# Optimization experiments

Measured on AMD Instinct MI355X. Metric: run time of the kernel, lower is better.

## Reference

```python
import jax, jax.numpy as jnp
import numpy as np

SCALE = 64 ** (-0.5)


def setup_inputs() -> dict:
    key = jax.random.key(0)
    ks = jax.random.split(key, 6)
    B, C, D, N = 2, 1024, 64, 128
    w_std = C ** (-0.5)
    return {
        "lidar": jax.random.normal(ks[0], (B, C, D, N), dtype=jnp.float32),
        "cam": jax.random.normal(ks[1], (B, C, D, N), dtype=jnp.float32),
        "Wq": jax.random.normal(ks[2], (C, C), dtype=jnp.float32) * w_std,
        "Wk": jax.random.normal(ks[3], (C, C), dtype=jnp.float32) * w_std,
        "Wv": jax.random.normal(ks[4], (C, C), dtype=jnp.float32) * w_std,
        "Wo": jax.random.normal(ks[5], (C, C), dtype=jnp.float32) * w_std,
    }


def _proj(W, x):
    # 1x1 Conv1d over flattened (D*N) positions == channel matmul, bias=False
    return jnp.einsum('oc,bcdn->bodn', W, x)


def reference(lidar, cam, Wq, Wk, Wv, Wo):
    q = _proj(Wq, lidar)  # [B, C, D, Ni]
    k = _proj(Wk, cam)    # [B, C, D, Nj]
    v = _proj(Wv, cam)    # [B, C, D, Nj]
    # contract over D (head-dim-like axis); scores per (batch, channel)
    dots = jnp.einsum('bhdi,bhdj->bhij', q, k) * SCALE  # [B, C, Ni, Nj]
    att = jax.nn.softmax(dots, axis=-1)
    # einsum 'a b i c,a b j c->a b j i': contract over cam positions
    out = jnp.einsum('bhic,bhjc->bhji', att, v)  # [B, C, D, Ni]
    out = jax.nn.gelu(_proj(Wo, out), approximate=False)
    return out
```

## Files before the change

kernel.cpp:

```cpp
#include <hip/hip_runtime.h>
#include <math.h>

#define CH  1024
#define PPB 8192

typedef __attribute__((ext_vector_type(8))) short short8;
typedef __attribute__((ext_vector_type(4))) float f32x4;

__device__ __forceinline__ ushort f2bf(float x) {
    uint u = __float_as_uint(x);
    return (ushort)((u + 0x7FFFu + ((u >> 16) & 1u)) >> 16);
}
__device__ __forceinline__ float bf2f(ushort u) {
    return __uint_as_float(((uint)u) << 16);
}
__device__ __forceinline__ void gload16(const void* g, const void* l) {
    __builtin_amdgcn_global_load_lds((const __attribute__((address_space(1))) void*)g,
                                     (__attribute__((address_space(3))) void*)l, 16, 0, 0);
}

__global__ __launch_bounds__(256) void prep(const float* __restrict__ lidar,
                                            const float* __restrict__ cam,
                                            const float* __restrict__ Wq,
                                            const float* __restrict__ Wk,
                                            const float* __restrict__ Wv,
                                            const float* __restrict__ Wo,
                                            ushort* __restrict__ wdst,
                                            ushort* __restrict__ lidT,
                                            ushort* __restrict__ camT)
{
    __shared__ float T[64][65];
    const int blk = blockIdx.x;
    const int tid = threadIdx.x;

    if (blk < 2048) {
        const int y = blk >> 9;
        const int x = blk & 511;
        const float* w = (y == 0) ? Wq : (y == 1) ? Wk : (y == 2) ? Wv : Wo;
        ushort* o = wdst + (size_t)y * (1u << 20);
        const int idx = (x * 256 + tid) * 8;
        const float4 v0 = *(const float4*)(w + idx);
        const float4 v1 = *(const float4*)(w + idx + 4);
        ushort4 o0, o1;
        o0.x = f2bf(v0.x); o0.y = f2bf(v0.y); o0.z = f2bf(v0.z); o0.w = f2bf(v0.w);
        o1.x = f2bf(v1.x); o1.y = f2bf(v1.y); o1.z = f2bf(v1.z); o1.w = f2bf(v1.w);
        *(ushort4*)(o + idx)     = o0;
        *(ushort4*)(o + idx + 4) = o1;
        return;
    }

    const int t = blk - 2048;
    const bool isLid = (t < 4096);
    const int tt = isLid ? t : t - 4096;
    const float* in = isLid ? lidar : cam;
    ushort* out = isLid ? lidT : camT;

    const int p0 = (tt & 127) * 64;
    const int c0 = ((tt >> 7) & 15) * 64;
    const int b  = tt >> 11;
    const int rc = tid >> 4;
    const int rp = (tid & 15) * 4;

    #pragma unroll
    for (int pass = 0; pass < 4; ++pass) {
        const int c = pass * 16 + rc;
        const size_t base = ((size_t)(b * CH + c0 + c)) * PPB + p0 + rp;
        const float4 v = *(const float4*)(in + base);
        T[c][rp] = v.x; T[c][rp + 1] = v.y; T[c][rp + 2] = v.z; T[c][rp + 3] = v.w;
    }
    __syncthreads();
    #pragma unroll
    for (int pass = 0; pass < 4; ++pass) {
        const int p = pass * 16 + rc;
        ushort4 o;
        o.x = f2bf(T[rp + 0][p]); o.y = f2bf(T[rp + 1][p]);
        o.z = f2bf(T[rp + 2][p]); o.w = f2bf(T[rp + 3][p]);
        *(ushort4*)(out + ((size_t)(b * PPB + p0 + p)) * CH + c0 + rp) = o;
    }
}

__global__ __launch_bounds__(256) void transpose_ao(const ushort* __restrict__ in_,
                                                    ushort* __restrict__ out)
{
    __shared__ float T[64][65];
    const int p0 = blockIdx.x * 64;
    const int c0 = blockIdx.y * 64;
    const int b  = blockIdx.z;
    const int t  = threadIdx.x;
    const int rc = t >> 4;
    const int rp = (t & 15) * 4;

    #pragma unroll
    for (int pass = 0; pass < 4; ++pass) {
        const int c = pass * 16 + rc;
        const size_t base = ((size_t)(b * CH + c0 + c)) * PPB + p0 + rp;
        const ushort4 v = *(const ushort4*)(in_ + base);
        T[c][rp]     = bf2f(v.x); T[c][rp + 1] = bf2f(v.y);
        T[c][rp + 2] = bf2f(v.z); T[c][rp + 3] = bf2f(v.w);
    }
    __syncthreads();
    #pragma unroll
    for (int pass = 0; pass < 4; ++pass) {
        const int p = pass * 16 + rc;
        const int prow = p * 128 + blockIdx.x;
        ushort4 o;
        o.x = f2bf(T[rp + 0][p]); o.y = f2bf(T[rp + 1][p]);
        o.z = f2bf(T[rp + 2][p]); o.w = f2bf(T[rp + 3][p]);
        *(ushort4*)(out + ((size_t)(b * PPB + prow)) * CH + c0 + rp) = o;
    }
}

__global__ __launch_bounds__(256) void gemm_qkv(const ushort* __restrict__ W3,
                                                const ushort* __restrict__ lidT,
                                                const ushort* __restrict__ camT,
                                                ushort* __restrict__ out3)
{
    __shared__ ushort As[2][128 * 32];
    __shared__ ushort Bs[2][128 * 32];

    const int bid = blockIdx.x;
    const int sid = (bid & 7) * 384 + (bid >> 3);
    const int g   = sid >> 10;
    const int r0  = sid & 1023;
    const int bm  = r0 & 7;
    const int bn  = r0 >> 3;
    const int m0  = bm * 128;
    const int n0g = bn * 128;
    const int b   = bn >> 6;
    const int p0  = (bn & 63) * 128;
    const int i0  = (bn & 63) * 2;

    const ushort* A  = W3 + (size_t)g * (1u << 20);
    const ushort* Bt = (g == 0) ? lidT : camT;
    const bool remap = (g < 2);
    ushort* Cout = out3 + (size_t)g * ((size_t)16 << 20);

    const int tid = threadIdx.x;
    const int w   = tid >> 6;
    const int l   = tid & 63;
    const int wr  = w >> 1, wc = w & 1;

    f32x4 acc[4][4];
    #pragma unroll
    for (int i = 0; i < 4; ++i)
        #pragma unroll
        for (int j = 0; j < 4; ++j) acc[i][j] = (f32x4)(0.0f);

    auto stage = [&](int buf, int kt) {
        const int k0 = kt * 32;
        #pragma unroll
        for (int i = 0; i < 2; ++i) {
            const int c  = w * 2 + i;
            const int rr = c * 16 + (l >> 2);
            const int ke = k0 + (l & 3) * 8;
            gload16(A + (size_t)(m0 + rr) * CH + ke, &As[buf][c * 512]);
            size_t brow;
            if (remap) brow = (size_t)b * PPB + (size_t)(rr & 63) * 128 + i0 + (rr >> 6);
            else       brow = (size_t)(n0g + rr);
            gload16(Bt + brow * CH + ke, &Bs[buf][c * 512]);
        }
    };

    stage(0, 0);
    int buf = 0;
    const int ks = (l >> 4) * 8;
    const int fr = l & 15;
    for (int kt = 0; kt < 32; ++kt) {
        __syncthreads();
        if (kt + 1 < 32) stage(buf ^ 1, kt + 1);
        short8 af[4], bfr[4];
        #pragma unroll
        for (int fm = 0; fm < 4; ++fm)
            af[fm] = *reinterpret_cast<const short8*>(
                &As[buf][(wr * 64 + fm * 16 + fr) * 32 + ks]);
        #pragma unroll
        for (int fn = 0; fn < 4; ++fn)
            bfr[fn] = *reinterpret_cast<const short8*>(
                &Bs[buf][(wc * 64 + fn * 16 + fr) * 32 + ks]);
        #pragma unroll
        for (int fm = 0; fm < 4; ++fm)
            #pragma unroll
            for (int fn = 0; fn < 4; ++fn)
                acc[fm][fn] = __builtin_amdgcn_mfma_f32_16x16x32_bf16(
                    af[fm], bfr[fn], acc[fm][fn], 0, 0, 0);
        buf ^= 1;
    }

    const int rq = l >> 4;
    #pragma unroll
    for (int fm = 0; fm < 4; ++fm)
        #pragma unroll
        for (int fn = 0; fn < 4; ++fn)
            #pragma unroll
            for (int r = 0; r < 4; ++r) {
                const int m = m0 + wr * 64 + fm * 16 + rq * 4 + r;
                const int n = wc * 64 + fn * 16 + fr;
                const size_t off = (size_t)b * CH * PPB + (size_t)m * PPB + p0 + n;
                ((ushort*)Cout)[off] = f2bf(acc[fm][fn][r]);
            }
}

__global__ __launch_bounds__(256) void gemm_wo(const ushort* __restrict__ A,
                                               const ushort* __restrict__ Bt,
                                               float* __restrict__ Cout)
{
    __shared__ ushort As[2][128 * 32];
    __shared__ ushort Bs[2][128 * 32];

    const int bid = blockIdx.x;
    const int sid = (bid & 7) * 128 + (bid >> 3);
    const int bm  = sid & 7;
    const int bn  = sid >> 3;
    const int m0  = bm * 128;
    const int n0g = bn * 128;
    const int b   = bn >> 6;
    const int p0  = (bn & 63) * 128;

    const int tid = threadIdx.x;
    const int w   = tid >> 6;
    const int l   = tid & 63;
    const int wr  = w >> 1, wc = w & 1;

    f32x4 acc[4][4];
    #pragma unroll
    for (int i = 0; i < 4; ++i)
        #pragma unroll
        for (int j = 0; j < 4; ++j) acc[i][j] = (f32x4)(0.0f);

    auto stage = [&](int buf, int kt) {
        const int k0 = kt * 32;
        #pragma unroll
        for (int i = 0; i < 2; ++i) {
            const int c  = w * 2 + i;
            const int rr = c * 16 + (l >> 2);
            const int ke = k0 + (l & 3) * 8;
            gload16(A  + (size_t)(m0 + rr) * CH + ke, &As[buf][c * 512]);
            gload16(Bt + (size_t)(n0g + rr) * CH + ke, &Bs[buf][c * 512]);
        }
    };

    stage(0, 0);
    int buf = 0;
    const int ks = (l >> 4) * 8;
    const int fr = l & 15;
    for (int kt = 0; kt < 32; ++kt) {
        __syncthreads();
        if (kt + 1 < 32) stage(buf ^ 1, kt + 1);
        short8 af[4], bfr[4];
        #pragma unroll
        for (int fm = 0; fm < 4; ++fm)
            af[fm] = *reinterpret_cast<const short8*>(
                &As[buf][(wr * 64 + fm * 16 + fr) * 32 + ks]);
        #pragma unroll
        for (int fn = 0; fn < 4; ++fn)
            bfr[fn] = *reinterpret_cast<const short8*>(
                &Bs[buf][(wc * 64 + fn * 16 + fr) * 32 + ks]);
        #pragma unroll
        for (int fm = 0; fm < 4; ++fm)
            #pragma unroll
            for (int fn = 0; fn < 4; ++fn)
                acc[fm][fn] = __builtin_amdgcn_mfma_f32_16x16x32_bf16(
                    af[fm], bfr[fn], acc[fm][fn], 0, 0, 0);
        buf ^= 1;
    }

    const int rq = l >> 4;
    #pragma unroll
    for (int fm = 0; fm < 4; ++fm)
        #pragma unroll
        for (int fn = 0; fn < 4; ++fn)
            #pragma unroll
            for (int r = 0; r < 4; ++r) {
                const int m = m0 + wr * 64 + fm * 16 + rq * 4 + r;
                const int n = wc * 64 + fn * 16 + fr;
                const float vv = acc[fm][fn][r];
                const size_t off = (size_t)b * CH * PPB + (size_t)m * PPB + p0 + n;
                Cout[off] = 0.5f * vv * (1.0f + erff(vv * 0.70710678118654752f));
            }
}

__global__ __launch_bounds__(256, 2) void attn_mfma(const ushort* __restrict__ qt,
                                                    const ushort* __restrict__ kt,
                                                    const ushort* __restrict__ vn,
                                                    ushort* __restrict__ ot)
{
    __shared__ ushort Qs[8192];
    __shared__ ushort Ks[8192];
    __shared__ ushort Vs[8192];
    __shared__ ushort Ps[16384];

    const int bh  = blockIdx.x;
    const int tid = threadIdx.x;
    const int w   = tid >> 6;
    const int l   = tid & 63;
    const int hi  = l >> 4;
    const int fr  = l & 15;
    const size_t base = (size_t)bh * 8192;

    {
        const int lr = l >> 3, lb = l & 7;
        const int vr = l >> 4, vbk = l & 15;
        #pragma unroll
        for (int q = 0; q < 4; ++q) {
            const int ch = w * 4 + q;
            const int i  = ch * 8 + lr;
            gload16(qt + base + i * 64 + ((lb ^ (i & 7)) << 3), &Qs[ch * 512]);
            gload16(kt + base + i * 64 + ((lb ^ (i & 7)) << 3), &Ks[ch * 512]);
            const int d  = ch * 4 + vr;
            gload16(vn + base + d * 128 + ((vbk ^ (d & 15)) << 3), &Vs[ch * 512]);
        }
    }
    __syncthreads();

    const int i0w = w * 32;
    f32x4 accS[2][8];
    #pragma unroll
    for (int a = 0; a < 2; ++a)
        #pragma unroll
        for (int bjj = 0; bjj < 8; ++bjj) accS[a][bjj] = (f32x4)(0.0f);

    #pragma unroll
    for (int kk = 0; kk < 2; ++kk) {
        const int blk = kk * 4 + hi;
        short8 aq[2];
        #pragma unroll
        for (int fm = 0; fm < 2; ++fm) {
            const int i = i0w + fm * 16 + fr;
            aq[fm] = *(const short8*)&Qs[i * 64 + ((blk ^ (i & 7)) << 3)];
        }
        #pragma unroll
        for (int fn = 0; fn < 8; ++fn) {
            const int j = fn * 16 + fr;
            const short8 bk = *(const short8*)&Ks[j * 64 + ((blk ^ (j & 7)) << 3)];
            #pragma unroll
            for (int fm = 0; fm < 2; ++fm)
                accS[fm][fn] = __builtin_amdgcn_mfma_f32_16x16x32_bf16(
                    aq[fm], bk, accS[fm][fn], 0, 0, 0);
        }
    }

    const float CS = 0.125f * 1.44269504088896341f;
    #pragma unroll
    for (int fm = 0; fm < 2; ++fm) {
        #pragma unroll
        for (int r = 0; r < 4; ++r) {
            float mx = accS[fm][0][r];
            #pragma unroll
            for (int fn = 1; fn < 8; ++fn) mx = fmaxf(mx, accS[fm][fn][r]);
            #pragma unroll
            for (int msk = 1; msk <= 8; msk <<= 1) mx = fmaxf(mx, __shfl_xor(mx, msk, 64));
            float e[8], sum = 0.f;
            #pragma unroll
            for (int fn = 0; fn < 8; ++fn) {
                e[fn] = exp2f((accS[fm][fn][r] - mx) * CS);
                sum += e[fn];
            }
            #pragma unroll
            for (int msk = 1; msk <= 8; msk <<= 1) sum += __shfl_xor(sum, msk, 64);
            const float is = 1.0f / sum;
            const int i = i0w + fm * 16 + hi * 4 + r;
            #pragma unroll
            for (int fn = 0; fn < 8; ++fn) {
                const int j = fn * 16 + fr;
                Ps[i * 128 + (((j >> 3) ^ (i & 15)) << 3) + (j & 7)] = f2bf(e[fn] * is);
            }
        }
    }

    f32x4 accO[2][4];
    #pragma unroll
    for (int a = 0; a < 2; ++a)
        #pragma unroll
        for (int bjj = 0; bjj < 4; ++bjj) accO[a][bjj] = (f32x4)(0.0f);

    #pragma unroll
    for (int ks2 = 0; ks2 < 4; ++ks2) {
        const int blk = ks2 * 4 + hi;
        short8 ap[2];
        #pragma unroll
        for (int fm = 0; fm < 2; ++fm) {
            const int i = i0w + fm * 16 + fr;
            ap[fm] = *(const short8*)&Ps[i * 128 + ((blk ^ (i & 15)) << 3)];
        }
        #pragma unroll
        for (int fn2 = 0; fn2 < 4; ++fn2) {
            const int d = fn2 * 16 + fr;
            const short8 bv = *(const short8*)&Vs[d * 128 + ((blk ^ (d & 15)) << 3)];
            #pragma unroll
            for (int fm = 0; fm < 2; ++fm)
                accO[fm][fn2] = __builtin_amdgcn_mfma_f32_16x16x32_bf16(
                    ap[fm], bv, accO[fm][fn2], 0, 0, 0);
        }
    }

    #pragma unroll
    for (int fm = 0; fm < 2; ++fm)
        #pragma unroll
        for (int fn2 = 0; fn2 < 4; ++fn2)
            #pragma unroll
            for (int r = 0; r < 4; ++r) {
                const int i = i0w + fm * 16 + hi * 4 + r;
                const int d = fn2 * 16 + fr;
                ot[base + i * 64 + d] = f2bf(accO[fm][fn2][r]);
            }
}

extern "C" void kernel_launch(void* const* d_in, const int* in_sizes, int n_in,
                              void* d_out, int out_size, void* d_ws, size_t ws_size,
                              hipStream_t stream)
{
    const float* lidar = (const float*)d_in[0];
    const float* cam   = (const float*)d_in[1];
    const float* Wq    = (const float*)d_in[2];
    const float* Wk    = (const float*)d_in[3];
    const float* Wv    = (const float*)d_in[4];
    const float* Wo    = (const float*)d_in[5];

    ushort* ws = (ushort*)d_ws;
    const size_t M1 = (size_t)1 << 20;
    const size_t TT = (size_t)16 << 20;
    ushort* Wob  = ws + 3 * M1;
    ushort* lidT = ws + 4 * M1;
    ushort* camT = lidT + TT;
    ushort* qb   = camT + TT;
    ushort* aoT  = lidT;

    const dim3 blk(256);
    prep<<<dim3(10240), blk, 0, stream>>>(lidar, cam, Wq, Wk, Wv, Wo, ws, lidT, camT);

    gemm_qkv<<<dim3(3072), blk, 0, stream>>>(ws, lidT, camT, qb);

    attn_mfma<<<dim3(2048), blk, 0, stream>>>(qb, qb + TT, qb + 2 * TT, qb);

    transpose_ao<<<dim3(128, 16, 2), blk, 0, stream>>>(qb, aoT);

    gemm_wo<<<dim3(1024), blk, 0, stream>>>(Wob, aoT, (float*)d_out);
}
```

Measured before the change: 289.8 us.

## Replace both projection GEMMs with a 256x256-tile swizzled, software-pipelined MFMA kernel

After: 268.3 us. 7.4% less time.

```diff
diff --git a/kernel.cpp b/kernel.cpp
--- a/kernel.cpp
+++ b/kernel.cpp
@@ -110,172 +110,147 @@
     }
 }
 
-__global__ __launch_bounds__(256) void gemm_qkv(const ushort* __restrict__ W3,
-                                                const ushort* __restrict__ lidT,
-                                                const ushort* __restrict__ camT,
-                                                ushort* __restrict__ out3)
+template <int IS_WO>
+__global__ __launch_bounds__(512, 2) void gemm256(const ushort* __restrict__ W3,
+                                                  const ushort* __restrict__ lidT,
+                                                  const ushort* __restrict__ camT,
+                                                  void* __restrict__ outp)
 {
-    __shared__ ushort As[2][128 * 32];
-    __shared__ ushort Bs[2][128 * 32];
+    __shared__ __align__(16) ushort sh[65536];
+    char* shb = (char*)sh;
 
     const int bid = blockIdx.x;
-    const int sid = (bid & 7) * 384 + (bid >> 3);
-    const int g   = sid >> 10;
-    const int r0  = sid & 1023;
-    const int bm  = r0 & 7;
-    const int bn  = r0 >> 3;
-    const int m0  = bm * 128;
-    const int n0g = bn * 128;
-    const int b   = bn >> 6;
-    const int p0  = (bn & 63) * 128;
-    const int i0  = (bn & 63) * 2;
-
+    int g, bm, bn;
+    if (IS_WO) {
+        const int sid = (bid & 7) * 32 + (bid >> 3);
+        g = 3; bm = sid & 3; bn = sid >> 2;
+    } else {
+        const int sid = (bid & 7) * 96 + (bid >> 3);
+        g = sid >> 8; const int r = sid & 255; bm = r & 3; bn = r >> 2;
+    }
+    const int m0  = bm * 256;
+    const int b   = bn >> 5;
+    const int nn0 = (bn & 31) * 4;
+    const int n0  = bn * 256;
     const ushort* A  = W3 + (size_t)g * (1u << 20);
     const ushort* Bt = (g == 0) ? lidT : camT;
-    const bool remap = (g < 2);
-    ushort* Cout = out3 + (size_t)g * ((size_t)16 << 20);
+    const bool remap = (!IS_WO) && (g < 2);
 
     const int tid = threadIdx.x;
     const int w   = tid >> 6;
     const int l   = tid & 63;
-    const int wr  = w >> 1, wc = w & 1;
-
-    f32x4 acc[4][4];
-    #pragma unroll
-    for (int i = 0; i < 4; ++i)
+    const int wr  = w >> 2;
+    const int wc  = w & 3;
+    const int hi  = l >> 4;
+    const int fr  = l & 15;
+
+    auto stageA = [&](int buf, int kt, int half) {
+        const int k0 = kt * 64;
+        #pragma unroll
+        for (int ld = 0; ld < 2; ++ld) {
+            const int c  = w * 2 + ld;
+            const int rt = half * 128 + c * 8 + (l >> 3);
+            const int kc = ((l & 7) ^ (rt & 7)) << 3;
+            gload16(A + (size_t)(m0 + rt) * CH + k0 + kc,
+                    &shb[buf * 32768 + half * 16384 + c * 1024]);
+        }
+    };
+    auto stageB = [&](int buf, int kt, int half) {
+        const int k0 = kt * 64;
+        #pragma unroll
+        for (int ld = 0; ld < 2; ++ld) {
+            const int c  = w * 2 + ld;
+            const int rt = half * 128 + c * 8 + (l >> 3);
+            const int kc = ((l & 7) ^ (rt & 7)) << 3;
+            size_t brow;
+            if (remap) brow = (size_t)b * PPB + (size_t)(rt & 63) * 128 + nn0 + (rt >> 6);
+            else       brow = (size_t)(n0 + rt);
+            gload16(Bt + brow * CH + k0 + kc,
+                    &shb[65536 + buf * 32768 + half * 16384 + c * 1024]);
+        }
+    };
+
+    f32x4 acc[8][4];
+    #pragma unroll
+    for (int i = 0; i < 8; ++i)
         #pragma unroll
         for (int j = 0; j < 4; ++j) acc[i][j] = (f32x4)(0.0f);
 
-    auto stage = [&](int buf, int kt) {
-        const int k0 = kt * 32;
-        #pragma unroll
-        for (int i = 0; i < 2; ++i) {
-            const int c  = w * 2 + i;
-            const int rr = c * 16 + (l >> 2);
-            const int ke = k0 + (l & 3) * 8;
-            gload16(A + (size_t)(m0 + rr) * CH + ke, &As[buf][c * 512]);
-            size_t brow;
-            if (remap) brow = (size_t)b * PPB + (size_t)(rr & 63) * 128 + i0 + (rr >> 6);
-            else       brow = (size_t)(n0g + rr);
-            gload16(Bt + brow * CH + ke, &Bs[buf][c * 512]);
-        }
-    };
-
-    stage(0, 0);
-    int buf = 0;
-    const int ks = (l >> 4) * 8;
-    const int fr = l & 15;
-    for (int kt = 0; kt < 32; ++kt) {
-        __syncthreads();
-        if (kt + 1 < 32) stage(buf ^ 1, kt + 1);
-        short8 af[4], bfr[4];
-        #pragma unroll
-        for (int fm = 0; fm < 4; ++fm)
-            af[fm] = *reinterpret_cast<const short8*>(
-                &As[buf][(wr * 64 + fm * 16 + fr) * 32 + ks]);
+    stageA(0, 0, 0); stageA(0, 0, 1); stageB(0, 0, 0); stageB(0, 0, 1);
+
+    for (int kt = 0; kt < 16; ++kt) {
+        const int buf = kt & 1, nxt = buf ^ 1;
+        if (kt < 15) {
+            stageA(nxt, kt + 1, 0);
+            __builtin_amdgcn_sched_barrier(0);
+            asm volatile("s_waitcnt vmcnt(2)" ::: "memory");
+        } else {
+            __builtin_amdgcn_sched_barrier(0);
+            asm volatile("s_waitcnt vmcnt(0)" ::: "memory");
+        }
+        __builtin_amdgcn_s_barrier();
+        __builtin_amdgcn_sched_barrier(0);
+        const int Ab = buf * 32768, Bb = 65536 + buf * 32768;
+
+        #pragma unroll
+        for (int q = 0; q < 4; ++q) {
+            const int mh = q >> 1, nh = q & 1;
+            if (kt < 15) {
+                if (q == 1) stageA(nxt, kt + 1, 1);
+                else if (q == 2) stageB(nxt, kt + 1, 0);
+                else if (q == 3) stageB(nxt, kt + 1, 1);
+            }
+            short8 aq[4][2], bq[2][2];
+            #pragma unroll
+            for (int fm = 0; fm < 4; ++fm) {
+                const int row = wr * 128 + (mh * 4 + fm) * 16 + fr;
+                #pragma unroll
+                for (int kk = 0; kk < 2; ++kk)
+                    aq[fm][kk] = *(const short8*)&shb[Ab + row * 128 +
+                        ((((kk << 2) + hi) ^ (row & 7)) << 4)];
+            }
+            #pragma unroll
+            for (int fn = 0; fn < 2; ++fn) {
+                const int row = wc * 64 + (nh * 2 + fn) * 16 + fr;
+                #pragma unroll
+                for (int kk = 0; kk < 2; ++kk)
+                    bq[fn][kk] = *(const short8*)&shb[Bb + row * 128 +
+                        ((((kk << 2) + hi) ^ (row & 7)) << 4)];
+            }
+            __builtin_amdgcn_s_setprio(1);
+            #pragma unroll
+            for (int fm = 0; fm < 4; ++fm)
+                #pragma unroll
+                for (int fn = 0; fn < 2; ++fn)
+                    #pragma unroll
+                    for (int kk = 0; kk < 2; ++kk)
+                        acc[mh * 4 + fm][nh * 2 + fn] =
+                            __builtin_amdgcn_mfma_f32_16x16x32_bf16(
+                                aq[fm][kk], bq[fn][kk],
+                                acc[mh * 4 + fm][nh * 2 + fn], 0, 0, 0);
+            __builtin_amdgcn_s_setprio(0);
+        }
+        __builtin_amdgcn_sched_barrier(0);
+        asm volatile("s_waitcnt lgkmcnt(0)" ::: "memory");
+        __builtin_amdgcn_sched_barrier(0);
+        __builtin_amdgcn_s_barrier();
+    }
+
+    #pragma unroll
+    for (int fm = 0; fm < 8; ++fm)
         #pragma unroll
         for (int fn = 0; fn < 4; ++fn)
-            bfr[fn] = *reinterpret_cast<const short8*>(
-                &Bs[buf][(wc * 64 + fn * 16 + fr) * 32 + ks]);
-        #pragma unroll
-        for (int fm = 0; fm < 4; ++fm)
-            #pragma unroll
-            for (int fn = 0; fn < 4; ++fn)
-                acc[fm][fn] = __builtin_amdgcn_mfma_f32_16x16x32_bf16(
-                    af[fm], bfr[fn], acc[fm][fn], 0, 0, 0);
-        buf ^= 1;
-    }
-
-    const int rq = l >> 4;
-    #pragma unroll
-    for (int fm = 0; fm < 4; ++fm)
-        #pragma unroll
-        for (int fn = 0; fn < 4; ++fn)
             #pragma unroll
             for (int r = 0; r < 4; ++r) {
-                const int m = m0 + wr * 64 + fm * 16 + rq * 4 + r;
-                const int n = wc * 64 + fn * 16 + fr;
-                const size_t off = (size_t)b * CH * PPB + (size_t)m * PPB + p0 + n;
-                ((ushort*)Cout)[off] = f2bf(acc[fm][fn][r]);
-            }
-}
-
-__global__ __launch_bounds__(256) void gemm_wo(const ushort* __restrict__ A,
-                                               const ushort* __restrict__ Bt,
-                                               float* __restrict__ Cout)
-{
-    __shared__ ushort As[2][128 * 32];
-    __shared__ ushort Bs[2][128 * 32];
-
-    const int bid = blockIdx.x;
-    const int sid = (bid & 7) * 128 + (bid >> 3);
-    const int bm  = sid & 7;
-    const int bn  = sid >> 3;
-    const int m0  = bm * 128;
-    const int n0g = bn * 128;
-    const int b   = bn >> 6;
-    const int p0  = (bn & 63) * 128;
-
-    const int tid = threadIdx.x;
-    const int w   = tid >> 6;
-    const int l   = tid & 63;
-    const int wr  = w >> 1, wc = w & 1;
-
-    f32x4 acc[4][4];
-    #pragma unroll
-    for (int i = 0; i < 4; ++i)
-        #pragma unroll
-        for (int j = 0; j < 4; ++j) acc[i][j] = (f32x4)(0.0f);
-
-    auto stage = [&](int buf, int kt) {
-        const int k0 = kt * 32;
-        #pragma unroll
-        for (int i = 0; i < 2; ++i) {
-            const int c  = w * 2 + i;
-            const int rr = c * 16 + (l >> 2);
-            const int ke = k0 + (l & 3) * 8;
-            gload16(A  + (size_t)(m0 + rr) * CH + ke, &As[buf][c * 512]);
-            gload16(Bt + (size_t)(n0g + rr) * CH + ke, &Bs[buf][c * 512]);
-        }
-    };
-
-    stage(0, 0);
-    int buf = 0;
-    const int ks = (l >> 4) * 8;
-    const int fr = l & 15;
-    for (int kt = 0; kt < 32; ++kt) {
-        __syncthreads();
-        if (kt + 1 < 32) stage(buf ^ 1, kt + 1);
-        short8 af[4], bfr[4];
-        #pragma unroll
-        for (int fm = 0; fm < 4; ++fm)
-            af[fm] = *reinterpret_cast<const short8*>(
-                &As[buf][(wr * 64 + fm * 16 + fr) * 32 + ks]);
-        #pragma unroll
-        for (int fn = 0; fn < 4; ++fn)
-            bfr[fn] = *reinterpret_cast<const short8*>(
-                &Bs[buf][(wc * 64 + fn * 16 + fr) * 32 + ks]);
-        #pragma unroll
-        for (int fm = 0; fm < 4; ++fm)
-            #pragma unroll
-            for (int fn = 0; fn < 4; ++fn)
-                acc[fm][fn] = __builtin_amdgcn_mfma_f32_16x16x32_bf16(
-                    af[fm], bfr[fn], acc[fm][fn], 0, 0, 0);
-        buf ^= 1;
-    }
-
-    const int rq = l >> 4;
-    #pragma unroll
-    for (int fm = 0; fm < 4; ++fm)
-        #pragma unroll
-        for (int fn = 0; fn < 4; ++fn)
-            #pragma unroll
-            for (int r = 0; r < 4; ++r) {
-                const int m = m0 + wr * 64 + fm * 16 + rq * 4 + r;
-                const int n = wc * 64 + fn * 16 + fr;
+                const int m = m0 + wr * 128 + fm * 16 + hi * 4 + r;
+                const int s = (bn & 31) * 256 + wc * 64 + fn * 16 + fr;
                 const float vv = acc[fm][fn][r];
-                const size_t off = (size_t)b * CH * PPB + (size_t)m * PPB + p0 + n;
-                Cout[off] = 0.5f * vv * (1.0f + erff(vv * 0.70710678118654752f));
+                const size_t off = (size_t)b * CH * PPB + (size_t)m * PPB + s;
+                if (IS_WO) {
+                    ((float*)outp)[off] = 0.5f * vv * (1.0f + erff(vv * 0.70710678118654752f));
+                } else {
+                    ((ushort*)outp)[(size_t)g * ((size_t)16 << 20) + off] = f2bf(vv);
+                }
             }
 }
 
@@ -419,20 +394,18 @@
     ushort* ws = (ushort*)d_ws;
     const size_t M1 = (size_t)1 << 20;
     const size_t TT = (size_t)16 << 20;
-    ushort* Wob  = ws + 3 * M1;
     ushort* lidT = ws + 4 * M1;
     ushort* camT = lidT + TT;
     ushort* qb   = camT + TT;
     ushort* aoT  = lidT;
 
-    const dim3 blk(256);
-    prep<<<dim3(10240), blk, 0, stream>>>(lidar, cam, Wq, Wk, Wv, Wo, ws, lidT, camT);
-
-    gemm_qkv<<<dim3(3072), blk, 0, stream>>>(ws, lidT, camT, qb);
-
-    attn_mfma<<<dim3(2048), blk, 0, stream>>>(qb, qb + TT, qb + 2 * TT, qb);
-
-    transpose_ao<<<dim3(128, 16, 2), blk, 0, stream>>>(qb, aoT);
-
-    gemm_wo<<<dim3(1024), blk, 0, stream>>>(Wob, aoT, (float*)d_out);
-}
+    prep<<<dim3(10240), dim3(256), 0, stream>>>(lidar, cam, Wq, Wk, Wv, Wo, ws, lidT, camT);
+
+    gemm256<0><<<dim3(768), dim3(512), 0, stream>>>(ws, lidT, camT, qb);
+
+    attn_mfma<<<dim3(2048), dim3(256), 0, stream>>>(qb, qb + TT, qb + 2 * TT, qb);
+
+    transpose_ao<<<dim3(128, 16, 2), dim3(256), 0, stream>>>(qb, aoT);
+
+    gemm256<1><<<dim3(256), dim3(512), 0, stream>>>(ws, aoT, aoT, (float*)d_out);
+}
```
